# Performance work log

Hardware: AMD Instinct MI355X
Metric: run time of the kernel (lower is better)

The kernel has to match this reference:

```python
import jax, jax.numpy as jnp
import numpy as np

B, S, HID = 2, 1024, 1024
NH, CH, HD = 16, 32, 64          # standard heads, constitutional heads, head_dim
TRUST = 64


def setup_inputs() -> dict:
    key = jax.random.key(0)
    ks = jax.random.split(key, 16)
    g = lambda k, sh, sc: jax.random.normal(k, sh, dtype=jnp.float32) * sc
    w = 1.0 / np.sqrt(HID)
    inp = {
        'hidden_states': g(ks[0], (B, S, HID), 1.0),
        'attention_mask': g(ks[1], (B, 1, S, S), 1.0),
        'trust_scores': jax.random.uniform(ks[2], (B, TRUST), dtype=jnp.float32),
        'Wq': g(ks[3], (HID, HID), w), 'bq': jnp.zeros((HID,), jnp.float32),
        'Wk': g(ks[4], (HID, HID), w), 'bk': jnp.zeros((HID,), jnp.float32),
        'Wv': g(ks[5], (HID, HID), w), 'bv': jnp.zeros((HID,), jnp.float32),
        'Wcq': g(ks[6], (HID, CH * HD), w), 'bcq': jnp.zeros((CH * HD,), jnp.float32),
        'Wck': g(ks[7], (HID, CH * HD), w), 'bck': jnp.zeros((CH * HD,), jnp.float32),
        'Wcv': g(ks[8], (HID, CH * HD), w), 'bcv': jnp.zeros((CH * HD,), jnp.float32),
        'Wt': g(ks[9], (TRUST, NH), 1.0 / np.sqrt(TRUST)), 'bt': jnp.zeros((NH,), jnp.float32),
        'Wo': g(ks[10], (HID, HID), w), 'bo': jnp.zeros((HID,), jnp.float32),
    }
    return inp


def reference(hidden_states, attention_mask, trust_scores,
              Wq, bq, Wk, bk, Wv, bv,
              Wcq, bcq, Wck, bck, Wcv, bcv,
              Wt, bt, Wo, bo):
    x = hidden_states
    scale = 1.0 / np.sqrt(HD).astype(np.float32)

    # standard QKV -> [B, NH, S, HD]
    q = (x @ Wq + bq).reshape(B, S, NH, HD)
    k = (x @ Wk + bk).reshape(B, S, NH, HD)
    v = (x @ Wv + bv).reshape(B, S, NH, HD)
    scores = jnp.einsum('bqhd,bkhd->bhqk', q, k) * scale  # [B,NH,S,S]
    scores = scores + attention_mask                       # additive mask

    # constitutional QKV -> [B, CH, S, HD]
    cq = (x @ Wcq + bcq).reshape(B, S, CH, HD)
    ck = (x @ Wck + bck).reshape(B, S, CH, HD)
    const_scores = jnp.einsum('bqhd,bkhd->bhqk', cq, ck) * scale  # [B,CH,S,S]

    # trust weighting: [B,TRUST] -> [B,NH] broadcast over [S,S]
    tw = trust_scores @ Wt + bt
    scores = scores * tw[:, :, None, None]

    # combine: per-head scores + mean over constitutional heads
    combined = scores + jnp.mean(const_scores, axis=1, keepdims=True)
    probs = jax.nn.softmax(combined, axis=-1)  # dropout is identity in eval

    context = jnp.einsum('bhqk,bkhd->bqhd', probs, v).reshape(B, S, HID)
    output = context @ Wo + bo
    return output, probs


if __name__ == '__main__':
    out, probs = reference(**setup_inputs())
    print(out.shape, probs.shape)
```

## Files before the change

### kernel.cpp

```cpp
#include <hip/hip_runtime.h>


typedef __bf16 bf16x8 __attribute__((ext_vector_type(8)));
typedef float  f32x4  __attribute__((ext_vector_type(4)));

static constexpr int Sq  = 1024;
static constexpr int LDP = 7168;

template<int ROWS>
__device__ __forceinline__ void stage_g(const __bf16* g, int ld, __bf16* s, int tid)
{
    constexpr int PER = (ROWS * 4) / 256;
    int w = tid >> 6, l = tid & 63;
#pragma unroll
    for (int i = 0; i < PER; i++) {
        int bc = w * 64 + i * 256;
        int chunk = bc + l;
        int row = chunk >> 2, part = (chunk & 3) * 8;
        const __bf16* gp = g + (size_t)row * ld + part;
        __bf16* sp = s + (size_t)bc * 8;
        __builtin_amdgcn_global_load_lds(
            (__attribute__((address_space(1))) void*)(gp),
            (__attribute__((address_space(3))) void*)(sp), 16, 0, 0);
    }
}

template<int BM, int BN, int EPI>
__global__ __launch_bounds__(256) void gemm_nt(
    const __bf16* __restrict__ A, int lda,
    const __bf16* __restrict__ B, int ldb,
    void* __restrict__ Cout, int ldc,
    const float* __restrict__ bias, int Ksz, float alpha)
{
    constexpr int WM = BM / 2, WN = BN / 2, FM = WM / 16, FN = WN / 16;
    __shared__ __bf16 As[BM][32];
    __shared__ __bf16 Bs[BN][32];
    int tid = threadIdx.x;
    int w = tid >> 6, l = tid & 63;
    int wr = w >> 1, wc = w & 1;
    int lr = l & 15, kp = (l >> 4) * 8;
    int bm = blockIdx.x * BM, bn = blockIdx.y * BN;
    int z = blockIdx.z;

    size_t zA = 0, zC = 0;
    if constexpr (EPI == 2) { zA = (size_t)z * 1024 * LDP; zC = (size_t)z * Sq * Sq; }

    f32x4 acc[FM][FN];
#pragma unroll
    for (int i = 0; i < FM; i++)
#pragma unroll
        for (int j = 0; j < FN; j++) acc[i][j] = (f32x4){0.f, 0.f, 0.f, 0.f};

    for (int k0 = 0; k0 < Ksz; k0 += 32) {
        stage_g<BM>(A + zA + (size_t)bm * lda + k0, lda, &As[0][0], tid);
        stage_g<BN>(B + zA + (size_t)bn * ldb + k0, ldb, &Bs[0][0], tid);
        __syncthreads();
        bf16x8 av[FM], bv[FN];
#pragma unroll
        for (int i = 0; i < FM; i++) av[i] = *(const bf16x8*)&As[wr * WM + i * 16 + lr][kp];
#pragma unroll
        for (int j = 0; j < FN; j++) bv[j] = *(const bf16x8*)&Bs[wc * WN + j * 16 + lr][kp];
#pragma unroll
        for (int i = 0; i < FM; i++)
#pragma unroll
            for (int j = 0; j < FN; j++)
                acc[i][j] = __builtin_amdgcn_mfma_f32_16x16x32_bf16(av[i], bv[j], acc[i][j], 0, 0, 0);
        __syncthreads();
    }

    int dr = (l >> 4) * 4, dc = l & 15;
#pragma unroll
    for (int i = 0; i < FM; i++)
#pragma unroll
        for (int j = 0; j < FN; j++)
#pragma unroll
            for (int t = 0; t < 4; t++) {
                int row = bm + wr * WM + i * 16 + dr + t;
                int col = bn + wc * WN + j * 16 + dc;
                float v = acc[i][j][t];
                size_t off = zC + (size_t)row * ldc + col;
                if constexpr (EPI == 0)      ((__bf16*)Cout)[off] = (__bf16)(v + bias[col]);
                else if constexpr (EPI == 1) ((float*)Cout)[off]  = v + bias[col];
                else                         ((float*)Cout)[off]  = v * alpha;
            }
}

__global__ __launch_bounds__(256) void attn_fused(
    const __bf16* __restrict__ PROJ, const __bf16* __restrict__ Vt,
    const float* __restrict__ mask, const float* __restrict__ CM,
    const float* __restrict__ TW, float* __restrict__ probs,
    __bf16* __restrict__ CTXb)
{
    __shared__ __bf16 Ps[32][1024];
    __shared__ float  red[32][4];
    __shared__ float  ctxred[2][16][64];

    int tid = threadIdx.x;
    int w = tid >> 6, l = tid & 63;
    int lr = l & 15, kp = (l >> 4) * 8;
    int dr = (l >> 4) * 4, dc = l & 15;
    int bm = blockIdx.x * 32;
    int z = blockIdx.y, b = z >> 4, h = z & 15;

    const __bf16* Qg = PROJ + (size_t)(b * 1024 + bm) * LDP + h * 64;
    const __bf16* Kg = PROJ + (size_t)(b * 1024) * LDP + 1024 + h * 64;

    bf16x8 av[2][2];
#pragma unroll
    for (int i = 0; i < 2; i++)
#pragma unroll
        for (int kk = 0; kk < 2; kk++)
            av[i][kk] = *(const bf16x8*)(Qg + (size_t)(i * 16 + lr) * LDP + kk * 32 + kp);

    f32x4 acc[2][16];
#pragma unroll
    for (int i = 0; i < 2; i++)
#pragma unroll
        for (int j = 0; j < 16; j++) acc[i][j] = (f32x4){0.f, 0.f, 0.f, 0.f};

#pragma unroll
    for (int j = 0; j < 16; j++) {
        const __bf16* Kt = Kg + (size_t)(w * 256 + j * 16 + lr) * LDP;
        bf16x8 b0 = *(const bf16x8*)(Kt + kp);
        bf16x8 b1 = *(const bf16x8*)(Kt + 32 + kp);
#pragma unroll
        for (int i = 0; i < 2; i++) {
            acc[i][j] = __builtin_amdgcn_mfma_f32_16x16x32_bf16(av[i][0], b0, acc[i][j], 0, 0, 0);
            acc[i][j] = __builtin_amdgcn_mfma_f32_16x16x32_bf16(av[i][1], b1, acc[i][j], 0, 0, 0);
        }
    }

    float twv = TW[z];
    const float* Mb  = mask + (size_t)b * Sq * Sq;
    const float* CMb = CM   + (size_t)b * Sq * Sq;

    float pm[2][4];
#pragma unroll
    for (int i = 0; i < 2; i++)
#pragma unroll
        for (int t = 0; t < 4; t++) pm[i][t] = -1e30f;

#pragma unroll
    for (int i = 0; i < 2; i++)
#pragma unroll
        for (int t = 0; t < 4; t++) {
            size_t rb = (size_t)(bm + i * 16 + dr + t) * 1024;
#pragma unroll
            for (int j = 0; j < 16; j++) {
                int col = w * 256 + j * 16 + dc;
                float lv = (acc[i][j][t] * 0.125f + Mb[rb + col]) * twv + CMb[rb + col];
                acc[i][j][t] = lv;
                pm[i][t] = fmaxf(pm[i][t], lv);
            }
        }
#pragma unroll
    for (int i = 0; i < 2; i++)
#pragma unroll
        for (int t = 0; t < 4; t++) {
#pragma unroll
            for (int off = 1; off < 16; off <<= 1) pm[i][t] = fmaxf(pm[i][t], __shfl_xor(pm[i][t], off));
        }
    if (dc == 0)
#pragma unroll
        for (int i = 0; i < 2; i++)
#pragma unroll
            for (int t = 0; t < 4; t++) red[i * 16 + dr + t][w] = pm[i][t];
    __syncthreads();
    float m8[2][4];
#pragma unroll
    for (int i = 0; i < 2; i++)
#pragma unroll
        for (int t = 0; t < 4; t++) {
            int r = i * 16 + dr + t;
            m8[i][t] = fmaxf(fmaxf(red[r][0], red[r][1]), fmaxf(red[r][2], red[r][3]));
        }

    float ps[2][4] = {};
#pragma unroll
    for (int i = 0; i < 2; i++)
#pragma unroll
        for (int t = 0; t < 4; t++) {
#pragma unroll
            for (int j = 0; j < 16; j++) {
                float e = __expf(acc[i][j][t] - m8[i][t]);
                acc[i][j][t] = e;
                ps[i][t] += e;
            }
#pragma unroll
            for (int off = 1; off < 16; off <<= 1) ps[i][t] += __shfl_xor(ps[i][t], off);
        }
    __syncthreads();
    if (dc == 0)
#pragma unroll
        for (int i = 0; i < 2; i++)
#pragma unroll
            for (int t = 0; t < 4; t++) red[i * 16 + dr + t][w] = ps[i][t];
    __syncthreads();

    float inv[2][4];
#pragma unroll
    for (int i = 0; i < 2; i++)
#pragma unroll
        for (int t = 0; t < 4; t++) {
            int r = i * 16 + dr + t;
            inv[i][t] = 1.0f / (red[r][0] + red[r][1] + red[r][2] + red[r][3]);
        }

    float* Pg = probs + (size_t)z * Sq * Sq;
#pragma unroll
    for (int i = 0; i < 2; i++)
#pragma unroll
        for (int t = 0; t < 4; t++) {
            int row = i * 16 + dr + t;
            size_t rb = (size_t)(bm + row) * 1024;
#pragma unroll
            for (int j = 0; j < 16; j++) {
                int col = w * 256 + j * 16 + dc;
                float p = acc[i][j][t] * inv[i][t];
                Pg[rb + col] = p;
                *(__bf16*)((char*)&Ps[0][0] + ((row * 2048 + col * 2) ^ ((row & 7) << 4))) = (__bf16)p;
            }
        }
    __syncthreads();

    int i3 = w & 1, kh = w >> 1;
    const __bf16* Vg = Vt + ((size_t)b * 1024 + h * 64) * 1024;
    f32x4 c2[4];
#pragma unroll
    for (int nt = 0; nt < 4; nt++) c2[nt] = (f32x4){0.f, 0.f, 0.f, 0.f};

    int arow = i3 * 16 + lr;
#pragma unroll
    for (int s = 0; s < 16; s++) {
        int k0 = kh * 512 + s * 32 + kp;
        bf16x8 a = *(const bf16x8*)((char*)&Ps[0][0] + ((arow * 2048 + k0 * 2) ^ ((arow & 7) << 4)));
#pragma unroll
        for (int nt = 0; nt < 4; nt++) {
            bf16x8 bv = *(const bf16x8*)(Vg + (size_t)(nt * 16 + lr) * 1024 + k0);
            c2[nt] = __builtin_amdgcn_mfma_f32_16x16x32_bf16(a, bv, c2[nt], 0, 0, 0);
        }
    }
    if (kh)
#pragma unroll
        for (int nt = 0; nt < 4; nt++)
#pragma unroll
            for (int t = 0; t < 4; t++) ctxred[i3][dr + t][nt * 16 + dc] = c2[nt][t];
    __syncthreads();
    if (!kh) {
#pragma unroll
        for (int nt = 0; nt < 4; nt++)
#pragma unroll
            for (int t = 0; t < 4; t++) {
                float v = c2[nt][t] + ctxred[i3][dr + t][nt * 16 + dc];
                CTXb[(size_t)(b * 1024 + bm + i3 * 16 + dr + t) * 1024 + h * 64 + nt * 16 + dc] = (__bf16)v;
            }
    }
}

__global__ __launch_bounds__(256) void convert_f32_bf16(
    const float* __restrict__ src, __bf16* __restrict__ dst)
{
    int i = blockIdx.x * 256 + threadIdx.x;
    size_t base = (size_t)i * 8;
    float4 a = *(const float4*)(src + base);
    float4 b = *(const float4*)(src + base + 4);
    bf16x8 o;
    o[0] = (__bf16)a.x; o[1] = (__bf16)a.y; o[2] = (__bf16)a.z; o[3] = (__bf16)a.w;
    o[4] = (__bf16)b.x; o[5] = (__bf16)b.y; o[6] = (__bf16)b.z; o[7] = (__bf16)b.w;
    *(bf16x8*)(dst + base) = o;
}

__global__ __launch_bounds__(256) void transpose_f32_bf16(
    const float* __restrict__ src, __bf16* __restrict__ dst, int K, int N)
{
    __shared__ float t[32][33];
    int tx = threadIdx.x, ty = threadIdx.y;
    int n0 = blockIdx.x * 32, k0 = blockIdx.y * 32;
#pragma unroll
    for (int i = 0; i < 4; i++)
        t[ty + i * 8][tx] = src[(size_t)(k0 + ty + i * 8) * N + n0 + tx];
    __syncthreads();
#pragma unroll
    for (int i = 0; i < 4; i++)
        dst[(size_t)(n0 + ty + i * 8) * K + k0 + tx] = (__bf16)t[tx][ty + i * 8];
}

__global__ __launch_bounds__(256) void transpose_v(
    const __bf16* __restrict__ PROJ, __bf16* __restrict__ Vt)
{
    int b = blockIdx.z;
    __shared__ __bf16 t[32][33];
    int tx = threadIdx.x, ty = threadIdx.y;
    int s0 = blockIdx.x * 32, d0 = blockIdx.y * 32;
#pragma unroll
    for (int i = 0; i < 4; i++)
        t[ty + i * 8][tx] = PROJ[(size_t)(b * 1024 + s0 + ty + i * 8) * LDP + 2048 + d0 + tx];
    __syncthreads();
#pragma unroll
    for (int i = 0; i < 4; i++)
        Vt[(size_t)(b * 1024 + d0 + ty + i * 8) * 1024 + s0 + tx] = t[tx][ty + i * 8];
}

__global__ void pack_bias(const float* bq, const float* bk, const float* bv,
                          const float* bcq, const float* bck, float* ball)
{
    int i = blockIdx.x * 256 + threadIdx.x;
    if (i >= LDP) return;
    float v;
    if (i < 1024) v = bq[i];
    else if (i < 2048) v = bk[i - 1024];
    else if (i < 3072) v = bv[i - 2048];
    else if (i < 5120) v = bcq[i - 3072];
    else v = bck[i - 5120];
    ball[i] = v;
}

__global__ void tw_kernel(const float* __restrict__ trust, const float* __restrict__ Wt,
                          const float* __restrict__ bt, float* __restrict__ tw)
{
    int i = threadIdx.x;
    if (i >= 32) return;
    int b = i >> 4, h = i & 15;
    float s = bt[h];
    for (int k = 0; k < 64; k++) s += trust[b * 64 + k] * Wt[k * 16 + h];
    tw[i] = s;
}

extern "C" void kernel_launch(void* const* d_in, const int* in_sizes, int n_in,
                              void* d_out, int out_size, void* d_ws, size_t ws_size,
                              hipStream_t stream)
{
    (void)in_sizes; (void)n_in; (void)out_size; (void)ws_size;
    const float* x     = (const float*)d_in[0];
    const float* mask  = (const float*)d_in[1];
    const float* trust = (const float*)d_in[2];
    const float* Wq  = (const float*)d_in[3];  const float* bq  = (const float*)d_in[4];
    const float* Wk  = (const float*)d_in[5];  const float* bk  = (const float*)d_in[6];
    const float* Wv  = (const float*)d_in[7];  const float* bv  = (const float*)d_in[8];
    const float* Wcq = (const float*)d_in[9];  const float* bcq = (const float*)d_in[10];
    const float* Wck = (const float*)d_in[11]; const float* bck = (const float*)d_in[12];
    const float* Wt  = (const float*)d_in[15]; const float* bt  = (const float*)d_in[16];
    const float* Wo  = (const float*)d_in[17]; const float* bo  = (const float*)d_in[18];

    float* out   = (float*)d_out;
    float* probs = out + (size_t)2 * Sq * 1024;

    constexpr size_t MB = 1u << 20;
    char* w8 = (char*)d_ws;
    __bf16* xb   = (__bf16*)(w8 + 0 * MB);
    __bf16* Wall = (__bf16*)(w8 + 4 * MB);
    float*  ball = (float*) (w8 + 19 * MB);
    float*  TW   = (float*) (w8 + 19 * MB + 65536);
    __bf16* WoT  = (__bf16*)(w8 + 19 * MB + 131072);
    __bf16* PROJ = (__bf16*)(w8 + 22 * MB);
    __bf16* Vt   = (__bf16*)(w8 + 50 * MB);
    float*  CM   = (float*) (w8 + 54 * MB);
    __bf16* CTXb = (__bf16*)(w8 + 62 * MB);
    WoT  = (__bf16*)(w8 + 19 * MB + 131072);
    PROJ = (__bf16*)(w8 + 22 * MB);
    Vt   = (__bf16*)(w8 + 50 * MB);
    CM   = (float*) (w8 + 54 * MB);
    CTXb = (__bf16*)(w8 + 4 * MB);
    CTXb = (__bf16*)(w8 + 0 * MB);

    dim3 tb(32, 8);

    convert_f32_bf16<<<1024, 256, 0, stream>>>(x, xb);
    transpose_f32_bf16<<<dim3(32, 32), tb, 0, stream>>>(Wq,  Wall + (size_t)0 * 1024 * 1024, 1024, 1024);
    transpose_f32_bf16<<<dim3(32, 32), tb, 0, stream>>>(Wk,  Wall + (size_t)1 * 1024 * 1024, 1024, 1024);
    transpose_f32_bf16<<<dim3(32, 32), tb, 0, stream>>>(Wv,  Wall + (size_t)2 * 1024 * 1024, 1024, 1024);
    transpose_f32_bf16<<<dim3(64, 32), tb, 0, stream>>>(Wcq, Wall + (size_t)3 * 1024 * 1024, 1024, 2048);
    transpose_f32_bf16<<<dim3(64, 32), tb, 0, stream>>>(Wck, Wall + (size_t)5 * 1024 * 1024, 1024, 2048);
    transpose_f32_bf16<<<dim3(32, 32), tb, 0, stream>>>(Wo,  WoT, 1024, 1024);
    pack_bias<<<28, 256, 0, stream>>>(bq, bk, bv, bcq, bck, ball);
    tw_kernel<<<1, 64, 0, stream>>>(trust, Wt, bt, TW);

    gemm_nt<128, 128, 0><<<dim3(16, 56, 1), 256, 0, stream>>>(
        xb, 1024, Wall, 1024, PROJ, LDP, ball, 1024, 0.f);

    transpose_v<<<dim3(32, 32, 2), tb, 0, stream>>>(PROJ, Vt);

    gemm_nt<128, 64, 2><<<dim3(8, 16, 2), 256, 0, stream>>>(
        PROJ + 3072, LDP, PROJ + 5120, LDP, CM, 1024, nullptr, 2048, 0.00390625f);

    attn_fused<<<dim3(32, 32), 256, 0, stream>>>(PROJ, Vt, mask, CM, TW, probs, CTXb);

    gemm_nt<128, 128, 1><<<dim3(16, 8, 1), 256, 0, stream>>>(
        CTXb, 1024, WoT, 1024, out, 1024, bo, 1024, 0.f);
}
```

Baseline: 230.9 us.

## Compute transposed scores so probabilities feed PV MFMA directly from registers

Swaps the MFMA operands in the QK^T step so each lane holds four consecutive key columns of a query row. This allows vectorized float4 loads of mask and constitutional scores and float4 stores of probs. The bf16 probabilities stay in registers and feed a 16x16x16 MFMA for P·V, which removes the 64KB shared P buffer and its barrier. Each wave now covers its own quarter of the keys, so partial contexts are summed through a four-way shared reduction. This trades the LDS P staging for more registers and a larger ctxred buffer.

Result: slower. 248.1 us (+7.4%).

```diff
diff --git a/kernel.cpp b/kernel.cpp
--- a/kernel.cpp
+++ b/kernel.cpp
@@ -2,6 +2,7 @@
 
 
 typedef __bf16 bf16x8 __attribute__((ext_vector_type(8)));
+typedef __bf16 bf16x4 __attribute__((ext_vector_type(4)));
 typedef float  f32x4  __attribute__((ext_vector_type(4)));
 
 static constexpr int Sq  = 1024;
@@ -91,26 +92,24 @@
     const float* __restrict__ TW, float* __restrict__ probs,
     __bf16* __restrict__ CTXb)
 {
-    __shared__ __bf16 Ps[32][1024];
-    __shared__ float  red[32][4];
-    __shared__ float  ctxred[2][16][64];
+    __shared__ float ctxred[4][64][36];
+    __shared__ float red[32][4];
 
     int tid = threadIdx.x;
     int w = tid >> 6, l = tid & 63;
-    int lr = l & 15, kp = (l >> 4) * 8;
-    int dr = (l >> 4) * 4, dc = l & 15;
+    int lr = l & 15, g = l >> 4, kp = g * 8;
     int bm = blockIdx.x * 32;
     int z = blockIdx.y, b = z >> 4, h = z & 15;
 
     const __bf16* Qg = PROJ + (size_t)(b * 1024 + bm) * LDP + h * 64;
     const __bf16* Kg = PROJ + (size_t)(b * 1024) * LDP + 1024 + h * 64;
 
-    bf16x8 av[2][2];
+    bf16x8 qv[2][2];
 #pragma unroll
     for (int i = 0; i < 2; i++)
 #pragma unroll
         for (int kk = 0; kk < 2; kk++)
-            av[i][kk] = *(const bf16x8*)(Qg + (size_t)(i * 16 + lr) * LDP + kk * 32 + kp);
+            qv[i][kk] = *(const bf16x8*)(Qg + (size_t)(i * 16 + lr) * LDP + kk * 32 + kp);
 
     f32x4 acc[2][16];
 #pragma unroll
@@ -121,12 +120,12 @@
 #pragma unroll
     for (int j = 0; j < 16; j++) {
         const __bf16* Kt = Kg + (size_t)(w * 256 + j * 16 + lr) * LDP;
-        bf16x8 b0 = *(const bf16x8*)(Kt + kp);
-        bf16x8 b1 = *(const bf16x8*)(Kt + 32 + kp);
+        bf16x8 k0 = *(const bf16x8*)(Kt + kp);
+        bf16x8 k1 = *(const bf16x8*)(Kt + 32 + kp);
 #pragma unroll
         for (int i = 0; i < 2; i++) {
-            acc[i][j] = __builtin_amdgcn_mfma_f32_16x16x32_bf16(av[i][0], b0, acc[i][j], 0, 0, 0);
-            acc[i][j] = __builtin_amdgcn_mfma_f32_16x16x32_bf16(av[i][1], b1, acc[i][j], 0, 0, 0);
+            acc[i][j] = __builtin_amdgcn_mfma_f32_16x16x32_bf16(k0, qv[i][0], acc[i][j], 0, 0, 0);
+            acc[i][j] = __builtin_amdgcn_mfma_f32_16x16x32_bf16(k1, qv[i][1], acc[i][j], 0, 0, 0);
         }
     }
 
@@ -134,127 +133,113 @@
     const float* Mb  = mask + (size_t)b * Sq * Sq;
     const float* CMb = CM   + (size_t)b * Sq * Sq;
 
-    float pm[2][4];
-#pragma unroll
-    for (int i = 0; i < 2; i++)
-#pragma unroll
-        for (int t = 0; t < 4; t++) pm[i][t] = -1e30f;
-
-#pragma unroll
-    for (int i = 0; i < 2; i++)
-#pragma unroll
-        for (int t = 0; t < 4; t++) {
-            size_t rb = (size_t)(bm + i * 16 + dr + t) * 1024;
-#pragma unroll
-            for (int j = 0; j < 16; j++) {
-                int col = w * 256 + j * 16 + dc;
-                float lv = (acc[i][j][t] * 0.125f + Mb[rb + col]) * twv + CMb[rb + col];
+    float mx[2];
+#pragma unroll
+    for (int i = 0; i < 2; i++) {
+        size_t rb = (size_t)(bm + i * 16 + lr) * 1024;
+        float mm = -1e30f;
+#pragma unroll
+        for (int j = 0; j < 16; j++) {
+            int off = w * 256 + j * 16 + g * 4;
+            f32x4 mk = *(const f32x4*)(Mb + rb + off);
+            f32x4 c4 = *(const f32x4*)(CMb + rb + off);
+#pragma unroll
+            for (int t = 0; t < 4; t++) {
+                float lv = (acc[i][j][t] * 0.125f + mk[t]) * twv + c4[t];
                 acc[i][j][t] = lv;
-                pm[i][t] = fmaxf(pm[i][t], lv);
+                mm = fmaxf(mm, lv);
             }
         }
+        mm = fmaxf(mm, __shfl_xor(mm, 16));
+        mm = fmaxf(mm, __shfl_xor(mm, 32));
+        mx[i] = mm;
+    }
+    if (g == 0) { red[lr][w] = mx[0]; red[16 + lr][w] = mx[1]; }
+    __syncthreads();
+#pragma unroll
+    for (int i = 0; i < 2; i++) {
+        const float* r = red[i * 16 + lr];
+        mx[i] = fmaxf(fmaxf(r[0], r[1]), fmaxf(r[2], r[3]));
+    }
+
+    float sm[2];
+#pragma unroll
+    for (int i = 0; i < 2; i++) {
+        float s = 0.f;
+#pragma unroll
+        for (int j = 0; j < 16; j++)
+#pragma unroll
+            for (int t = 0; t < 4; t++) {
+                float e = __expf(acc[i][j][t] - mx[i]);
+                acc[i][j][t] = e;
+                s += e;
+            }
+        s += __shfl_xor(s, 16);
+        s += __shfl_xor(s, 32);
+        sm[i] = s;
+    }
+    __syncthreads();
+    if (g == 0) { red[lr][w] = sm[0]; red[16 + lr][w] = sm[1]; }
+    __syncthreads();
+
+    float* Pg = probs + (size_t)z * Sq * Sq;
+    bf16x4 pa[2][16];
+#pragma unroll
+    for (int i = 0; i < 2; i++) {
+        const float* r = red[i * 16 + lr];
+        float inv = 1.0f / (r[0] + r[1] + r[2] + r[3]);
+        size_t rb = (size_t)(bm + i * 16 + lr) * 1024;
+#pragma unroll
+        for (int j = 0; j < 16; j++) {
+            f32x4 p;
+#pragma unroll
+            for (int t = 0; t < 4; t++) p[t] = acc[i][j][t] * inv;
+            *(f32x4*)(Pg + rb + w * 256 + j * 16 + g * 4) = p;
+            bf16x4 q4;
+#pragma unroll
+            for (int t = 0; t < 4; t++) q4[t] = (__bf16)p[t];
+            pa[i][j] = q4;
+        }
+    }
+
+    const __bf16* Vg = Vt + ((size_t)b * 1024 + h * 64) * 1024;
+    f32x4 c[2][4];
 #pragma unroll
     for (int i = 0; i < 2; i++)
 #pragma unroll
-        for (int t = 0; t < 4; t++) {
-#pragma unroll
-            for (int off = 1; off < 16; off <<= 1) pm[i][t] = fmaxf(pm[i][t], __shfl_xor(pm[i][t], off));
-        }
-    if (dc == 0)
+        for (int nt = 0; nt < 4; nt++) c[i][nt] = (f32x4){0.f, 0.f, 0.f, 0.f};
+
+#pragma unroll
+    for (int j = 0; j < 16; j++) {
+        int kb = w * 256 + j * 16 + g * 4;
+        bf16x4 vb[4];
+#pragma unroll
+        for (int nt = 0; nt < 4; nt++)
+            vb[nt] = *(const bf16x4*)(Vg + (size_t)(nt * 16 + lr) * 1024 + kb);
 #pragma unroll
         for (int i = 0; i < 2; i++)
 #pragma unroll
-            for (int t = 0; t < 4; t++) red[i * 16 + dr + t][w] = pm[i][t];
-    __syncthreads();
-    float m8[2][4];
+            for (int nt = 0; nt < 4; nt++)
+                asm volatile("v_mfma_f32_16x16x16_bf16 %0, %1, %2, %0"
+                             : "+v"(c[i][nt]) : "v"(pa[i][j]), "v"(vb[nt]));
+    }
+
 #pragma unroll
     for (int i = 0; i < 2; i++)
 #pragma unroll
-        for (int t = 0; t < 4; t++) {
-            int r = i * 16 + dr + t;
-            m8[i][t] = fmaxf(fmaxf(red[r][0], red[r][1]), fmaxf(red[r][2], red[r][3]));
-        }
-
-    float ps[2][4] = {};
-#pragma unroll
-    for (int i = 0; i < 2; i++)
-#pragma unroll
-        for (int t = 0; t < 4; t++) {
-#pragma unroll
-            for (int j = 0; j < 16; j++) {
-                float e = __expf(acc[i][j][t] - m8[i][t]);
-                acc[i][j][t] = e;
-                ps[i][t] += e;
-            }
-#pragma unroll
-            for (int off = 1; off < 16; off <<= 1) ps[i][t] += __shfl_xor(ps[i][t], off);
-        }
-    __syncthreads();
-    if (dc == 0)
-#pragma unroll
-        for (int i = 0; i < 2; i++)
-#pragma unroll
-            for (int t = 0; t < 4; t++) red[i * 16 + dr + t][w] = ps[i][t];
-    __syncthreads();
-
-    float inv[2][4];
-#pragma unroll
-    for (int i = 0; i < 2; i++)
-#pragma unroll
-        for (int t = 0; t < 4; t++) {
-            int r = i * 16 + dr + t;
-            inv[i][t] = 1.0f / (red[r][0] + red[r][1] + red[r][2] + red[r][3]);
-        }
-
-    float* Pg = probs + (size_t)z * Sq * Sq;
-#pragma unroll
-    for (int i = 0; i < 2; i++)
-#pragma unroll
-        for (int t = 0; t < 4; t++) {
-            int row = i * 16 + dr + t;
-            size_t rb = (size_t)(bm + row) * 1024;
-#pragma unroll
-            for (int j = 0; j < 16; j++) {
-                int col = w * 256 + j * 16 + dc;
-                float p = acc[i][j][t] * inv[i][t];
-                Pg[rb + col] = p;
-                *(__bf16*)((char*)&Ps[0][0] + ((row * 2048 + col * 2) ^ ((row & 7) << 4))) = (__bf16)p;
-            }
-        }
-    __syncthreads();
-
-    int i3 = w & 1, kh = w >> 1;
-    const __bf16* Vg = Vt + ((size_t)b * 1024 + h * 64) * 1024;
-    f32x4 c2[4];
-#pragma unroll
-    for (int nt = 0; nt < 4; nt++) c2[nt] = (f32x4){0.f, 0.f, 0.f, 0.f};
-
-    int arow = i3 * 16 + lr;
-#pragma unroll
-    for (int s = 0; s < 16; s++) {
-        int k0 = kh * 512 + s * 32 + kp;
-        bf16x8 a = *(const bf16x8*)((char*)&Ps[0][0] + ((arow * 2048 + k0 * 2) ^ ((arow & 7) << 4)));
-#pragma unroll
-        for (int nt = 0; nt < 4; nt++) {
-            bf16x8 bv = *(const bf16x8*)(Vg + (size_t)(nt * 16 + lr) * 1024 + k0);
-            c2[nt] = __builtin_amdgcn_mfma_f32_16x16x32_bf16(a, bv, c2[nt], 0, 0, 0);
-        }
-    }
-    if (kh)
-#pragma unroll
         for (int nt = 0; nt < 4; nt++)
-#pragma unroll
-            for (int t = 0; t < 4; t++) ctxred[i3][dr + t][nt * 16 + dc] = c2[nt][t];
-    __syncthreads();
-    if (!kh) {
-#pragma unroll
-        for (int nt = 0; nt < 4; nt++)
-#pragma unroll
-            for (int t = 0; t < 4; t++) {
-                float v = c2[nt][t] + ctxred[i3][dr + t][nt * 16 + dc];
-                CTXb[(size_t)(b * 1024 + bm + i3 * 16 + dr + t) * 1024 + h * 64 + nt * 16 + dc] = (__bf16)v;
-            }
-    }
+            *(f32x4*)&ctxred[w][nt * 16 + lr][i * 16 + g * 4] = c[i][nt];
+    __syncthreads();
+
+    int q8 = tid & 31, dq = (tid >> 5) * 8;
+    bf16x8 o;
+#pragma unroll
+    for (int e = 0; e < 8; e++) {
+        int d = dq + e;
+        float s = ctxred[0][d][q8] + ctxred[1][d][q8] + ctxred[2][d][q8] + ctxred[3][d][q8];
+        o[e] = (__bf16)s;
+    }
+    *(bf16x8*)&CTXb[(size_t)(b * 1024 + bm + q8) * 1024 + h * 64 + dq] = o;
 }
 
 __global__ __launch_bounds__(256) void convert_f32_bf16(
@@ -355,13 +340,7 @@
     __bf16* PROJ = (__bf16*)(w8 + 22 * MB);
     __bf16* Vt   = (__bf16*)(w8 + 50 * MB);
     float*  CM   = (float*) (w8 + 54 * MB);
-    __bf16* CTXb = (__bf16*)(w8 + 62 * MB);
-    WoT  = (__bf16*)(w8 + 19 * MB + 131072);
-    PROJ = (__bf16*)(w8 + 22 * MB);
-    Vt   = (__bf16*)(w8 + 50 * MB);
-    CM   = (float*) (w8 + 54 * MB);
-    CTXb = (__bf16*)(w8 + 4 * MB);
-    CTXb = (__bf16*)(w8 + 0 * MB);
+    __bf16* CTXb = (__bf16*)(w8 + 0 * MB);
 
     dim3 tb(32, 8);
 
```
